# Performance work log

Measured on AMD Instinct MI355X. Metric: run time of the kernel, lower is better.

Reference implementation:

```python
import jax, jax.numpy as jnp
import numpy as np
from jax import lax

T, H, W = 2048, 128, 160


def setup_inputs() -> dict:
    key = jax.random.key(0)
    k1, = jax.random.split(key, 1)
    batch_x = jax.random.uniform(k1, (T, 1, H, W), dtype=jnp.float32)
    # params = [close, open, dhot] / 255 (defaults 1, 5, 8)
    params = jnp.array([1.0, 5.0, 8.0], dtype=jnp.float32) / 255.0
    HT0 = jnp.zeros((H, W), dtype=jnp.float32)
    LT0 = jnp.zeros((H, W), dtype=jnp.float32)
    # ConvTranspose2d(1,1,3,padding=1) with constant weight ones/(3**2/2) = 2/9;
    # symmetric kernel + padding=1 transposed conv == SAME-padded standard conv.
    kernel = jnp.full((1, 1, 3, 3), 2.0 / 9.0, dtype=jnp.float32)
    return {"batch_x": batch_x, "params": params, "HT0": HT0, "LT0": LT0, "kernel": kernel}


def reference(batch_x, params, HT0, LT0, kernel):
    d_close, d_open, d_hot = params[0], params[1], params[2]

    def step(carry, x):
        HT, LT = carry
        img = x[0]  # (H, W)
        # hot scores computed against *pre-update* thresholds
        tmpH_hot = jax.nn.sigmoid((img - HT - d_hot) * 500.0)
        tmpH = (img - HT) > 0
        HT = jnp.where(tmpH, HT + d_open, HT - d_close)
        tmpL_hot = jax.nn.sigmoid((LT - img - d_hot) * 500.0)
        tmpL = (LT - img) > 0
        LT = jnp.where(tmpL, LT - d_open, LT + d_close)
        return (HT, LT), tmpH_hot + tmpL_hot

    _, hot = lax.scan(step, (HT0, LT0), batch_x)  # hot: (T, H, W)

    # DiffErosion: relu(1 - conv(1 - x)) with SAME padding, batched over frames
    where_zero = (1.0 - hot)[:, None, :, :]  # (T, 1, H, W)
    sub = lax.conv_general_dilated(
        where_zero, kernel, window_strides=(1, 1), padding="SAME",
        dimension_numbers=("NCHW", "OIHW", "NCHW"))
    return jax.nn.relu(1.0 - sub)  # (T, 1, H, W)
```

## Files before the change

kernel.cpp:

```cpp
#include <hip/hip_runtime.h>


#define TILE_W 16
#define TILE_H 16
#define IN_W 14
#define IN_H 14
#define BUF 8
#define B32 32

constexpr int T_FRAMES = 2048;
constexpr int H_IMG = 128;
constexpr int W_IMG = 160;
constexpr int HW = H_IMG * W_IMG;
constexpr float C1 = 721.3475204444817f;

constexpr size_t ws_needed(int snap) {
    return (size_t)(T_FRAMES / snap - 1) * HW * sizeof(float2);
}

__device__ __forceinline__ float dpp_from_left(float v) {
    return __int_as_float(__builtin_amdgcn_update_dpp(0, __float_as_int(v), 0x111, 0xF, 0xF, true));
}
__device__ __forceinline__ float dpp_from_right(float v) {
    return __int_as_float(__builtin_amdgcn_update_dpp(0, __float_as_int(v), 0x101, 0xF, 0xF, true));
}

#define ISSUE_BATCH(V, F)                          \
    _Pragma("unroll")                              \
    for (int i = 0; i < B32; ++i) V[i] = xp[((F) + i) * HW];

#define COMP_BATCH(V)                              \
    _Pragma("unroll")                              \
    for (int i = 0; i < B32; ++i) {                \
        const float img = V[i];                    \
        HT = ((img - HT) > 0.0f) ? (HT + dO) : (HT - dC); \
        LT = ((LT - img) > 0.0f) ? (LT - dO) : (LT + dC); \
    }

#define SNAPSHOT(F)                                \
    if (((F) % SNAP_) == 0) {                      \
        const int k = (F) / SNAP_ - 1;             \
        if (k < T_FRAMES / SNAP_ - 1)              \
            snap[k * HW + pix] = make_float2(HT, LT); \
    }

template <int SNAP_>
__global__ __launch_bounds__(64, 1)
void svs_scan(const float* __restrict__ x, const float* __restrict__ params,
              const float* __restrict__ HT0, const float* __restrict__ LT0,
              float2* __restrict__ snap)
{
    const int pix = (int)blockIdx.x * 64 + (int)threadIdx.x;
    const float dC = params[0];
    const float dO = params[1];

    float HT = HT0[pix];
    float LT = LT0[pix];
    const float* xp = x + pix;

    float v0[B32], v1[B32], v2[B32], v3[B32];
    ISSUE_BATCH(v0, 0)
    ISSUE_BATCH(v1, B32)
    ISSUE_BATCH(v2, 2 * B32)
    ISSUE_BATCH(v3, 3 * B32)

    for (int t = 0; t < T_FRAMES; t += 4 * B32) {
        const bool more = (t + 4 * B32) < T_FRAMES;
        COMP_BATCH(v0)
        if (more) { ISSUE_BATCH(v0, t + 4 * B32) }
        COMP_BATCH(v1)
        SNAPSHOT(t + 2 * B32)
        if (more) { ISSUE_BATCH(v1, t + 5 * B32) }
        COMP_BATCH(v2)
        if (more) { ISSUE_BATCH(v2, t + 6 * B32) }
        COMP_BATCH(v3)
        SNAPSHOT(t + 4 * B32)
        if (more) { ISSUE_BATCH(v3, t + 7 * B32) }
    }
}

template <int SNAP_>
__global__ __launch_bounds__(256)
void svs_compute(const float* __restrict__ x, const float* __restrict__ params,
                 const float* __restrict__ HT0, const float* __restrict__ LT0,
                 const float* __restrict__ kern, const float2* __restrict__ snap,
                 float* __restrict__ out)
{
    constexpr int NSLICE_ = T_FRAMES / SNAP_;
    constexpr int TOTAL_ = 120 * NSLICE_;
    const int lin = (int)blockIdx.x + 12 * (int)blockIdx.y + 120 * (int)blockIdx.z;
    const int w   = (lin & 7) * (TOTAL_ / 8) + (lin >> 3);
    const int bx  = w % 12;
    const int by  = (w / 12) % 10;
    const int slice = w / 120;

    const int tx = threadIdx.x & 15;
    const int ty = threadIdx.x >> 4;
    const int gx = bx * IN_W + tx - 1;
    const int gy = by * IN_H + ty - 1;
    const int t0 = slice * SNAP_;

    const bool valid = (gx >= 0) & (gx < W_IMG) & (gy >= 0) & (gy < H_IMG);
    const int cx = min(max(gx, 0), W_IMG - 1);
    const int cy = min(max(gy, 0), H_IMG - 1);
    const int pix = cy * W_IMG + cx;

    const float dC   = params[0];
    const float dO   = params[1];
    const float dHot = params[2];
    const float kw   = kern[4];
    const float c0   = dHot * C1;

    float HT, LT;
    if (slice == 0) {
        HT = valid ? HT0[pix] : 0.0f;
        LT = valid ? LT0[pix] : 0.0f;
    } else {
        const float2 s = snap[(slice - 1) * HW + pix];
        HT = valid ? s.x : 0.0f;
        LT = valid ? s.y : 0.0f;
    }

    __shared__ float sm[TILE_H][BUF][TILE_W + 1];

    const bool doOut = (tx >= 1) & (tx <= IN_W) & (ty >= 1) & (ty <= IN_H) & valid;
    const int ym = max(ty - 1, 0);
    const int yp = min(ty + 1, TILE_H - 1);
    const float* xp = x + pix;
    float* op = out + pix;

    for (int tb = t0; tb < t0 + SNAP_; tb += BUF) {
        float v[BUF], hot[BUF];
        #pragma unroll
        for (int i = 0; i < BUF; ++i) v[i] = xp[(tb + i) * HW];
        #pragma unroll
        for (int i = 0; i < BUF; ++i) {
            const float img = v[i];
            const float aH = img - HT;
            const float eH = __builtin_amdgcn_exp2f(fmaf(aH, -C1, c0));
            const float hH = __builtin_amdgcn_rcpf(1.0f + eH);
            HT = (aH > 0.0f) ? (HT + dO) : (HT - dC);
            const float aL = LT - img;
            const float eL = __builtin_amdgcn_exp2f(fmaf(aL, -C1, c0));
            const float hL = __builtin_amdgcn_rcpf(1.0f + eL);
            LT = (aL > 0.0f) ? (LT - dO) : (LT + dC);
            hot[i] = valid ? (hH + hL) : 1.0f;
            sm[ty][i][tx] = hot[i];
        }
        __syncthreads();
        #pragma unroll
        for (int i = 0; i < BUF; ++i) {
            const float r0 = sm[ym][i][tx];
            const float r1 = sm[yp][i][tx];
            const float vs = r0 + hot[i] + r1;
            const float S  = vs + dpp_from_left(vs) + dpp_from_right(vs);
            float o = fmaf(S, kw, -1.0f);
            o = fmaxf(o, 0.0f);
            if (doOut) op[(tb + i) * HW] = o;
        }
        __syncthreads();
    }
}

#define NCHUNK 8
constexpr int CHUNK = T_FRAMES / NCHUNK;

__global__ __launch_bounds__(256)
void svs_fused(const float* __restrict__ x, const float* __restrict__ params,
               const float* __restrict__ HT0, const float* __restrict__ LT0,
               const float* __restrict__ kern, float* __restrict__ out)
{
    const int tx = threadIdx.x & 15;
    const int ty = threadIdx.x >> 4;
    const int gx = (int)blockIdx.x * IN_W + tx - 1;
    const int gy = (int)blockIdx.y * IN_H + ty - 1;
    const int chunk = (NCHUNK - 1) - (int)blockIdx.z;

    const bool valid = (gx >= 0) & (gx < W_IMG) & (gy >= 0) & (gy < H_IMG);
    const int cx = min(max(gx, 0), W_IMG - 1);
    const int cy = min(max(gy, 0), H_IMG - 1);
    const int pix = cy * W_IMG + cx;

    const float dC   = params[0];
    const float dO   = params[1];
    const float dHot = params[2];
    const float kw   = kern[4];

    float HT = valid ? HT0[pix] : 0.0f;
    float LT = valid ? LT0[pix] : 0.0f;

    const float* xp = x + pix;
    const int t0 = chunk * CHUNK;

    for (int t = 0; t < t0; t += BUF) {
        float v[BUF];
        #pragma unroll
        for (int i = 0; i < BUF; ++i) v[i] = xp[(t + i) * HW];
        #pragma unroll
        for (int i = 0; i < BUF; ++i) {
            const float img = v[i];
            HT = ((img - HT) > 0.0f) ? (HT + dO) : (HT - dC);
            LT = ((LT - img) > 0.0f) ? (LT - dO) : (LT + dC);
        }
    }

    __shared__ float sm[TILE_H][BUF][TILE_W + 1];
    const bool doOut = (tx >= 1) & (tx <= IN_W) & (ty >= 1) & (ty <= IN_H) & valid;
    const int ym = max(ty - 1, 0);
    const int yp = min(ty + 1, TILE_H - 1);
    const float c0 = dHot * C1;
    float* op = out + pix;

    for (int tb = t0; tb < t0 + CHUNK; tb += BUF) {
        float v[BUF], hot[BUF];
        #pragma unroll
        for (int i = 0; i < BUF; ++i) v[i] = xp[(tb + i) * HW];
        #pragma unroll
        for (int i = 0; i < BUF; ++i) {
            const float img = v[i];
            const float aH = img - HT;
            const float eH = __builtin_amdgcn_exp2f(fmaf(aH, -C1, c0));
            const float hH = __builtin_amdgcn_rcpf(1.0f + eH);
            HT = (aH > 0.0f) ? (HT + dO) : (HT - dC);
            const float aL = LT - img;
            const float eL = __builtin_amdgcn_exp2f(fmaf(aL, -C1, c0));
            const float hL = __builtin_amdgcn_rcpf(1.0f + eL);
            LT = (aL > 0.0f) ? (LT - dO) : (LT + dC);
            hot[i] = valid ? (hH + hL) : 1.0f;
            sm[ty][i][tx] = hot[i];
        }
        __syncthreads();
        #pragma unroll
        for (int i = 0; i < BUF; ++i) {
            const float r0 = sm[ym][i][tx];
            const float r1 = sm[yp][i][tx];
            const float vs = r0 + hot[i] + r1;
            const float S  = vs + dpp_from_left(vs) + dpp_from_right(vs);
            float o = fmaf(S, kw, -1.0f);
            o = fmaxf(o, 0.0f);
            if (doOut) op[(tb + i) * HW] = o;
        }
        __syncthreads();
    }
}

extern "C" void kernel_launch(void* const* d_in, const int* in_sizes, int n_in,
                              void* d_out, int out_size, void* d_ws, size_t ws_size,
                              hipStream_t stream) {
    const float* x      = (const float*)d_in[0];
    const float* params = (const float*)d_in[1];
    const float* HT0p   = (const float*)d_in[2];
    const float* LT0p   = (const float*)d_in[3];
    const float* kern   = (const float*)d_in[4];
    float* out = (float*)d_out;

    if (ws_size >= ws_needed(64)) {
        float2* snap = (float2*)d_ws;
        svs_scan<64><<<dim3(HW / 64), dim3(64), 0, stream>>>(x, params, HT0p, LT0p, snap);
        svs_compute<64><<<dim3(12, 10, T_FRAMES / 64), dim3(256), 0, stream>>>(
            x, params, HT0p, LT0p, kern, snap, out);
    } else if (ws_size >= ws_needed(128)) {
        float2* snap = (float2*)d_ws;
        svs_scan<128><<<dim3(HW / 64), dim3(64), 0, stream>>>(x, params, HT0p, LT0p, snap);
        svs_compute<128><<<dim3(12, 10, T_FRAMES / 128), dim3(256), 0, stream>>>(
            x, params, HT0p, LT0p, kern, snap, out);
    } else {
        dim3 grid((W_IMG + IN_W - 1) / IN_W, (H_IMG + IN_H - 1) / IN_H, NCHUNK);
        svs_fused<<<grid, dim3(256), 0, stream>>>(x, params, HT0p, LT0p, kern, out);
    }
}
```

Before: 153.0 us.

## Restructure scan prefetch to triple buffer, skip last slice, use 256-thread blocks

The threshold scan kernel now uses three rotating 32-frame register buffers with sched_barriers instead of four, and stops before the final SNAP-sized slice, whose state is never needed. Blocks grow from 64 to 256 threads, giving 80 blocks instead of 320. The fused fallback kernel is removed and replaced by svs_compute with a single slice, and snapshot indexing is widened to size_t. Reading fewer frames cuts HBM traffic in the serial scan, but fewer, larger blocks may spread less well across CUs and lower per-wave memory parallelism.

```diff
diff --git a/kernel.cpp b/kernel.cpp
--- a/kernel.cpp
+++ b/kernel.cpp
@@ -6,7 +6,7 @@
 #define IN_W 14
 #define IN_H 14
 #define BUF 8
-#define B32 32
+#define PRE 32
 
 constexpr int T_FRAMES = 2048;
 constexpr int H_IMG = 128;
@@ -25,32 +25,26 @@
     return __int_as_float(__builtin_amdgcn_update_dpp(0, __float_as_int(v), 0x101, 0xF, 0xF, true));
 }
 
-#define ISSUE_BATCH(V, F)                          \
+#define S_ISSUE(V, F)                              \
     _Pragma("unroll")                              \
-    for (int i = 0; i < B32; ++i) V[i] = xp[((F) + i) * HW];
+    for (int i = 0; i < PRE; ++i) V[i] = xp[((F) + i) * HW];
 
-#define COMP_BATCH(V)                              \
+#define S_COMP(V)                                  \
     _Pragma("unroll")                              \
-    for (int i = 0; i < B32; ++i) {                \
+    for (int i = 0; i < PRE; ++i) {                \
         const float img = V[i];                    \
         HT = ((img - HT) > 0.0f) ? (HT + dO) : (HT - dC); \
         LT = ((LT - img) > 0.0f) ? (LT - dO) : (LT + dC); \
     }
 
-#define SNAPSHOT(F)                                \
-    if (((F) % SNAP_) == 0) {                      \
-        const int k = (F) / SNAP_ - 1;             \
-        if (k < T_FRAMES / SNAP_ - 1)              \
-            snap[k * HW + pix] = make_float2(HT, LT); \
-    }
-
 template <int SNAP_>
-__global__ __launch_bounds__(64, 1)
+__global__ __launch_bounds__(256, 1)
 void svs_scan(const float* __restrict__ x, const float* __restrict__ params,
               const float* __restrict__ HT0, const float* __restrict__ LT0,
               float2* __restrict__ snap)
 {
-    const int pix = (int)blockIdx.x * 64 + (int)threadIdx.x;
+    constexpr int TEFF = T_FRAMES - SNAP_;
+    const int pix = (int)blockIdx.x * 256 + (int)threadIdx.x;
     const float dC = params[0];
     const float dO = params[1];
 
@@ -58,24 +52,36 @@
     float LT = LT0[pix];
     const float* xp = x + pix;
 
-    float v0[B32], v1[B32], v2[B32], v3[B32];
-    ISSUE_BATCH(v0, 0)
-    ISSUE_BATCH(v1, B32)
-    ISSUE_BATCH(v2, 2 * B32)
-    ISSUE_BATCH(v3, 3 * B32)
+    auto maybe_snap = [&](int endf) {
+        if ((endf % SNAP_) == 0) {
+            const int k = endf / SNAP_ - 1;
+            if (k < T_FRAMES / SNAP_ - 1)
+                snap[(size_t)k * HW + pix] = make_float2(HT, LT);
+        }
+    };
 
-    for (int t = 0; t < T_FRAMES; t += 4 * B32) {
-        const bool more = (t + 4 * B32) < T_FRAMES;
-        COMP_BATCH(v0)
-        if (more) { ISSUE_BATCH(v0, t + 4 * B32) }
-        COMP_BATCH(v1)
-        SNAPSHOT(t + 2 * B32)
-        if (more) { ISSUE_BATCH(v1, t + 5 * B32) }
-        COMP_BATCH(v2)
-        if (more) { ISSUE_BATCH(v2, t + 6 * B32) }
-        COMP_BATCH(v3)
-        SNAPSHOT(t + 4 * B32)
-        if (more) { ISSUE_BATCH(v3, t + 7 * B32) }
+    float va[PRE], vb[PRE], vc[PRE];
+    S_ISSUE(va, 0)
+    S_ISSUE(vb, PRE)
+    __builtin_amdgcn_sched_barrier(0);
+
+    for (int t = 0; t < TEFF; t += 3 * PRE) {
+        if (t + 2 * PRE < TEFF) { S_ISSUE(vc, t + 2 * PRE) }
+        __builtin_amdgcn_sched_barrier(0);
+        S_COMP(va)
+        maybe_snap(t + PRE);
+        if (t + 3 * PRE < TEFF) { S_ISSUE(va, t + 3 * PRE) }
+        __builtin_amdgcn_sched_barrier(0);
+        if (t + PRE < TEFF) {
+            S_COMP(vb)
+            maybe_snap(t + 2 * PRE);
+        }
+        if (t + 4 * PRE < TEFF) { S_ISSUE(vb, t + 4 * PRE) }
+        __builtin_amdgcn_sched_barrier(0);
+        if (t + 2 * PRE < TEFF) {
+            S_COMP(vc)
+            maybe_snap(t + 3 * PRE);
+        }
     }
 }
 
@@ -116,7 +122,7 @@
         HT = valid ? HT0[pix] : 0.0f;
         LT = valid ? LT0[pix] : 0.0f;
     } else {
-        const float2 s = snap[(slice - 1) * HW + pix];
+        const float2 s = snap[(size_t)(slice - 1) * HW + pix];
         HT = valid ? s.x : 0.0f;
         LT = valid ? s.y : 0.0f;
     }
@@ -162,88 +168,6 @@
     }
 }
 
-#define NCHUNK 8
-constexpr int CHUNK = T_FRAMES / NCHUNK;
-
-__global__ __launch_bounds__(256)
-void svs_fused(const float* __restrict__ x, const float* __restrict__ params,
-               const float* __restrict__ HT0, const float* __restrict__ LT0,
-               const float* __restrict__ kern, float* __restrict__ out)
-{
-    const int tx = threadIdx.x & 15;
-    const int ty = threadIdx.x >> 4;
-    const int gx = (int)blockIdx.x * IN_W + tx - 1;
-    const int gy = (int)blockIdx.y * IN_H + ty - 1;
-    const int chunk = (NCHUNK - 1) - (int)blockIdx.z;
-
-    const bool valid = (gx >= 0) & (gx < W_IMG) & (gy >= 0) & (gy < H_IMG);
-    const int cx = min(max(gx, 0), W_IMG - 1);
-    const int cy = min(max(gy, 0), H_IMG - 1);
-    const int pix = cy * W_IMG + cx;
-
-    const float dC   = params[0];
-    const float dO   = params[1];
-    const float dHot = params[2];
-    const float kw   = kern[4];
-
-    float HT = valid ? HT0[pix] : 0.0f;
-    float LT = valid ? LT0[pix] : 0.0f;
-
-    const float* xp = x + pix;
-    const int t0 = chunk * CHUNK;
-
-    for (int t = 0; t < t0; t += BUF) {
-        float v[BUF];
-        #pragma unroll
-        for (int i = 0; i < BUF; ++i) v[i] = xp[(t + i) * HW];
-        #pragma unroll
-        for (int i = 0; i < BUF; ++i) {
-            const float img = v[i];
-            HT = ((img - HT) > 0.0f) ? (HT + dO) : (HT - dC);
-            LT = ((LT - img) > 0.0f) ? (LT - dO) : (LT + dC);
-        }
-    }
-
-    __shared__ float sm[TILE_H][BUF][TILE_W + 1];
-    const bool doOut = (tx >= 1) & (tx <= IN_W) & (ty >= 1) & (ty <= IN_H) & valid;
-    const int ym = max(ty - 1, 0);
-    const int yp = min(ty + 1, TILE_H - 1);
-    const float c0 = dHot * C1;
-    float* op = out + pix;
-
-    for (int tb = t0; tb < t0 + CHUNK; tb += BUF) {
-        float v[BUF], hot[BUF];
-        #pragma unroll
-        for (int i = 0; i < BUF; ++i) v[i] = xp[(tb + i) * HW];
-        #pragma unroll
-        for (int i = 0; i < BUF; ++i) {
-            const float img = v[i];
-            const float aH = img - HT;
-            const float eH = __builtin_amdgcn_exp2f(fmaf(aH, -C1, c0));
-            const float hH = __builtin_amdgcn_rcpf(1.0f + eH);
-            HT = (aH > 0.0f) ? (HT + dO) : (HT - dC);
-            const float aL = LT - img;
-            const float eL = __builtin_amdgcn_exp2f(fmaf(aL, -C1, c0));
-            const float hL = __builtin_amdgcn_rcpf(1.0f + eL);
-            LT = (aL > 0.0f) ? (LT - dO) : (LT + dC);
-            hot[i] = valid ? (hH + hL) : 1.0f;
-            sm[ty][i][tx] = hot[i];
-        }
-        __syncthreads();
-        #pragma unroll
-        for (int i = 0; i < BUF; ++i) {
-            const float r0 = sm[ym][i][tx];
-            const float r1 = sm[yp][i][tx];
-            const float vs = r0 + hot[i] + r1;
-            const float S  = vs + dpp_from_left(vs) + dpp_from_right(vs);
-            float o = fmaf(S, kw, -1.0f);
-            o = fmaxf(o, 0.0f);
-            if (doOut) op[(tb + i) * HW] = o;
-        }
-        __syncthreads();
-    }
-}
-
 extern "C" void kernel_launch(void* const* d_in, const int* in_sizes, int n_in,
                               void* d_out, int out_size, void* d_ws, size_t ws_size,
                               hipStream_t stream) {
@@ -256,16 +180,16 @@
 
     if (ws_size >= ws_needed(64)) {
         float2* snap = (float2*)d_ws;
-        svs_scan<64><<<dim3(HW / 64), dim3(64), 0, stream>>>(x, params, HT0p, LT0p, snap);
+        svs_scan<64><<<dim3(HW / 256), dim3(256), 0, stream>>>(x, params, HT0p, LT0p, snap);
         svs_compute<64><<<dim3(12, 10, T_FRAMES / 64), dim3(256), 0, stream>>>(
             x, params, HT0p, LT0p, kern, snap, out);
     } else if (ws_size >= ws_needed(128)) {
         float2* snap = (float2*)d_ws;
-        svs_scan<128><<<dim3(HW / 64), dim3(64), 0, stream>>>(x, params, HT0p, LT0p, snap);
+        svs_scan<128><<<dim3(HW / 256), dim3(256), 0, stream>>>(x, params, HT0p, LT0p, snap);
         svs_compute<128><<<dim3(12, 10, T_FRAMES / 128), dim3(256), 0, stream>>>(
             x, params, HT0p, LT0p, kern, snap, out);
     } else {
-        dim3 grid((W_IMG + IN_W - 1) / IN_W, (H_IMG + IN_H - 1) / IN_H, NCHUNK);
-        svs_fused<<<grid, dim3(256), 0, stream>>>(x, params, HT0p, LT0p, kern, out);
+        svs_compute<2048><<<dim3(12, 10, 1), dim3(256), 0, stream>>>(
+            x, params, HT0p, LT0p, kern, (const float2*)d_ws, out);
     }
 }
```

Result: faster. 145.0 us, median of 2 (-5.3%).
